# Kernel optimization log

Measured on AMD Instinct MI355X. Metric: run time of the kernel, lower is better.

## Reference

```python
import jax, jax.numpy as jnp
import numpy as np

D_MODEL = 1024

def setup_inputs() -> dict:
    key = jax.random.key(0)
    ks = jax.random.split(key, 7)
    x = jax.random.normal(ks[0], (4, 2048, D_MODEL), dtype=jnp.float32)
    s = 1.0 / np.sqrt(D_MODEL)
    Wq = jax.random.uniform(ks[1], (D_MODEL, D_MODEL), jnp.float32, -s, s)
    bq = jax.random.uniform(ks[2], (D_MODEL,), jnp.float32, -s, s)
    Wk = jax.random.uniform(ks[3], (D_MODEL, D_MODEL), jnp.float32, -s, s)
    bk = jax.random.uniform(ks[4], (D_MODEL,), jnp.float32, -s, s)
    Wv = jax.random.uniform(ks[5], (D_MODEL, D_MODEL), jnp.float32, -s, s)
    bv = jax.random.uniform(ks[6], (D_MODEL,), jnp.float32, -s, s)
    return {"x": x, "Wq": Wq, "bq": bq, "Wk": Wk, "bk": bk, "Wv": Wv, "bv": bv}

def reference(x, Wq, bq, Wk, bk, Wv, bv):
    # single-head self-attention: q,k,v are [B, S, D]
    q = x @ Wq + bq
    k = x @ Wk + bk
    v = x @ Wv + bv
    scale = 1.0 / jnp.sqrt(jnp.asarray(D_MODEL, x.dtype))
    scores = jnp.einsum('bsd,btd->bst', q, k) * scale  # [B, S, S]
    attn = jax.nn.softmax(scores, axis=-1)
    return jnp.einsum('bst,btd->bsd', attn, v)
```

## Files before the change

### kernel.cpp

```cpp
#include <hip/hip_runtime.h>
#include <hip/hip_bf16.h>
#include <stdint.h>


typedef __attribute__((ext_vector_type(8))) short short8;
typedef __attribute__((ext_vector_type(4))) float f32x4;

__device__ __forceinline__ unsigned short f2bf(float f) {
  union { float f; uint32_t u; } c; c.f = f;
  uint32_t u = c.u;
  u += 0x7FFFu + ((u >> 16) & 1u);
  return (unsigned short)(u >> 16);
}

__device__ __forceinline__ void gl16(const void* g, void* l) {
  __builtin_amdgcn_global_load_lds(
      (const __attribute__((address_space(1))) unsigned int*)g,
      (__attribute__((address_space(3))) unsigned int*)l, 16, 0, 0);
}

template <int EPI>
__global__ __launch_bounds__(256) void gemm_bt(
    const short* __restrict__ A, int lda, long sAz,
    const short* __restrict__ B, int ldb, long sBz,
    void* __restrict__ Cv, int ldc, long sCz,
    int K, float scale,
    const float* __restrict__ bias0, const float* __restrict__ bias1,
    const float* __restrict__ bias2, float* __restrict__ rowsum)
{
  __shared__ short lds[18432];
  short* sA = lds;
  short* sB = lds + 8192;

  const int tid  = threadIdx.x;
  const int lane = tid & 63;
  const int wid  = tid >> 6;
  const int z    = blockIdx.z;
  const long tileM = (long)blockIdx.y * 128;
  const long tileN = (long)blockIdx.x * 128;
  const short* Az = A + (long)z * sAz;
  const short* Bz = B + (long)z * sBz;

  const int r0 = wid * 16 + (lane >> 2);
  const int c0 = (lane & 3) * 8;
  const short* gA0 = Az + (tileM + r0) * lda + c0;
  const short* gB0 = Bz + (tileN + r0) * ldb + c0;
  short* lA0 = sA + (wid * 64 + lane) * 8;
  short* lB0 = sB + (wid * 64 + lane) * 8;
  const long a64 = 64L * lda, b64 = 64L * ldb;

  const int fr = lane & 15, quad = lane >> 4;
  const int waveM = (wid >> 1) * 64, waveN = (wid & 1) * 64;

  f32x4 acc[4][4] = {};

  for (int kt = 0; kt < K; kt += 64) {
    __syncthreads();
    gl16(gA0 + kt,             lA0);
    gl16(gA0 + kt + a64,       lA0 + 2048);
    gl16(gA0 + kt + 32,        lA0 + 4096);
    gl16(gA0 + kt + a64 + 32,  lA0 + 6144);
    gl16(gB0 + kt,             lB0);
    gl16(gB0 + kt + b64,       lB0 + 2048);
    gl16(gB0 + kt + 32,        lB0 + 4096);
    gl16(gB0 + kt + b64 + 32,  lB0 + 6144);
    __syncthreads();

#pragma unroll
    for (int kk = 0; kk < 2; ++kk) {
      short8 af[4], bf[4];
#pragma unroll
      for (int i = 0; i < 4; ++i)
        af[i] = *(const short8*)&sA[kk * 4096 + (waveM + i * 16 + fr) * 32 + quad * 8];
#pragma unroll
      for (int j = 0; j < 4; ++j)
        bf[j] = *(const short8*)&sB[kk * 4096 + (waveN + j * 16 + fr) * 32 + quad * 8];
#pragma unroll
      for (int i = 0; i < 4; ++i)
#pragma unroll
        for (int j = 0; j < 4; ++j)
          acc[i][j] = __builtin_amdgcn_mfma_f32_16x16x32_bf16(af[i], bf[j],
                                                              acc[i][j], 0, 0, 0);
    }
  }

  if (EPI == 1) {
#pragma unroll
    for (int i = 0; i < 4; ++i)
#pragma unroll
      for (int j = 0; j < 4; ++j)
#pragma unroll
        for (int r = 0; r < 4; ++r)
          acc[i][j][r] = exp2f(acc[i][j][r] * scale);
#pragma unroll
    for (int i = 0; i < 4; ++i)
#pragma unroll
      for (int r = 0; r < 4; ++r) {
        float s = acc[i][0][r] + acc[i][1][r] + acc[i][2][r] + acc[i][3][r];
        s += __shfl_xor(s, 1);
        s += __shfl_xor(s, 2);
        s += __shfl_xor(s, 4);
        s += __shfl_xor(s, 8);
        if (fr == 0)
          atomicAdd(&rowsum[(long)z * 2048 + tileM + waveM + i * 16 + quad * 4 + r], s);
      }
  }

  if (EPI <= 1) {
    __syncthreads();
    short* scr = lds + wid * 4608;
    short* C = (short*)Cv + (long)z * sCz;
    const float* bias = (z == 0) ? bias0 : ((z == 1) ? bias1 : bias2);
#pragma unroll
    for (int j = 0; j < 4; ++j) {
      const float bv = (EPI == 0) ? bias[tileN + waveN + j * 16 + fr] : 0.0f;
#pragma unroll
      for (int i = 0; i < 4; ++i)
#pragma unroll
        for (int r = 0; r < 4; ++r)
          scr[(i * 16 + quad * 4 + r) * 72 + j * 16 + fr] =
              (short)f2bf(acc[i][j][r] + bv);
    }
    __syncthreads();
#pragma unroll
    for (int c = 0; c < 8; ++c) {
      const int row = c * 8 + (lane >> 3);
      const int col = (lane & 7) * 8;
      short8 v = *(const short8*)&scr[row * 72 + col];
      *(short8*)(C + (tileM + waveM + row) * ldc + tileN + waveN + col) = v;
    }
  } else {
    float* C = (float*)Cv + (long)z * sCz;
#pragma unroll
    for (int i = 0; i < 4; ++i)
#pragma unroll
      for (int r = 0; r < 4; ++r) {
        const long gr = tileM + waveM + i * 16 + quad * 4 + r;
        const float rinv = 1.0f / rowsum[(long)z * 2048 + gr];
#pragma unroll
        for (int j = 0; j < 4; ++j)
          C[gr * ldc + tileN + waveN + j * 16 + fr] = acc[i][j][r] * rinv;
      }
  }
}

__global__ __launch_bounds__(256) void cvt_f32_to_bf16(
    const float4* __restrict__ x, ushort4* __restrict__ y)
{
  const long i = (long)blockIdx.x * 256 + threadIdx.x;
  float4 v = x[i];
  ushort4 o;
  o.x = f2bf(v.x); o.y = f2bf(v.y); o.z = f2bf(v.z); o.w = f2bf(v.w);
  y[i] = o;
}

__global__ __launch_bounds__(256) void transpose_cvt_w(
    const float* __restrict__ Wq, const float* __restrict__ Wk,
    const float* __restrict__ Wv, short* __restrict__ WT)
{
  __shared__ short tile[32][33];
  const int z = blockIdx.z;
  const float* W = (z == 0) ? Wq : ((z == 1) ? Wk : Wv);
  short* d = WT + (long)z * 1024 * 1024;
  const int n0 = blockIdx.x * 32, d0 = blockIdx.y * 32;
  const int tx = threadIdx.x & 31, ty = threadIdx.x >> 5;
#pragma unroll
  for (int p = 0; p < 4; ++p)
    tile[ty + p * 8][tx] = (short)f2bf(W[(long)(d0 + ty + p * 8) * 1024 + n0 + tx]);
  __syncthreads();
#pragma unroll
  for (int p = 0; p < 4; ++p)
    d[(long)(n0 + ty + p * 8) * 1024 + d0 + tx] = tile[tx][ty + p * 8];
}

__global__ __launch_bounds__(256) void transpose_bf16(
    const short* __restrict__ src, short* __restrict__ dst)
{
  __shared__ short tile[32][33];
  const int z = blockIdx.z;
  const int d0 = blockIdx.x * 32, t0 = blockIdx.y * 32;
  const int tx = threadIdx.x & 31, ty = threadIdx.x >> 5;
  const short* s = src + (long)z * 2048 * 1024;
  short* d = dst + (long)z * 1024 * 2048;
#pragma unroll
  for (int p = 0; p < 4; ++p)
    tile[ty + p * 8][tx] = s[(long)(t0 + ty + p * 8) * 1024 + d0 + tx];
  __syncthreads();
#pragma unroll
  for (int p = 0; p < 4; ++p)
    d[(long)(d0 + ty + p * 8) * 2048 + t0 + tx] = tile[tx][ty + p * 8];
}

extern "C" void kernel_launch(void* const* d_in, const int* in_sizes, int n_in,
                              void* d_out, int out_size, void* d_ws, size_t ws_size,
                              hipStream_t stream) {
  const float* x  = (const float*)d_in[0];
  const float* Wq = (const float*)d_in[1];
  const float* bq = (const float*)d_in[2];
  const float* Wk = (const float*)d_in[3];
  const float* bk = (const float*)d_in[4];
  const float* Wv = (const float*)d_in[5];
  const float* bv = (const float*)d_in[6];

  char* ws = (char*)d_ws;
  short* xb  = (short*)(ws);
  short* wt  = (short*)(ws + 16777216);
  short* qkv = (short*)(ws + 23068672);
  short* Pp  = (short*)(ws + 73400320);
  float* rs  = (float*)(ws + 106954752);
  short* vT  = xb;

  hipMemsetAsync(rs, 0, 4 * 2048 * sizeof(float), stream);
  cvt_f32_to_bf16<<<8192, 256, 0, stream>>>((const float4*)x, (ushort4*)xb);
  transpose_cvt_w<<<dim3(32, 32, 3), 256, 0, stream>>>(Wq, Wk, Wv, wt);
  gemm_bt<0><<<dim3(8, 64, 3), 256, 0, stream>>>(
      xb, 1024, 0L, wt, 1024, 1048576L, qkv, 1024, 8388608L,
      1024, 1.0f, bq, bk, bv, nullptr);
  transpose_bf16<<<dim3(32, 64, 4), 256, 0, stream>>>(qkv + 2L * 8388608, vT);
  gemm_bt<1><<<dim3(16, 16, 4), 256, 0, stream>>>(
      qkv, 1024, 2097152L, qkv + 8388608, 1024, 2097152L, Pp, 2048, 4194304L,
      1024, 0.03125f * 1.44269504088896f, nullptr, nullptr, nullptr, rs);
  gemm_bt<2><<<dim3(8, 16, 4), 256, 0, stream>>>(
      Pp, 2048, 4194304L, vT, 2048, 2097152L, d_out, 1024, 2097152L,
      2048, 1.0f, nullptr, nullptr, nullptr, rs);
}
```

Baseline: 299.2 us.

## Double-buffer GEMM LDS tiles and fuse prep kernels into one launch

Restructures the shared GEMM main loop to use two 32-wide K tiles in LDS. The global-to-LDS load for the next tile is issued before the MFMA work on the current one, so each iteration needs only one barrier and load latency can overlap compute. The float-to-bf16 conversion of x, the weight transpose-convert and the rowsum zeroing (previously a memset) are merged into a single prep launch to cut launch overhead. A per-wave epilogue barrier is also dropped. The price is twice as many K iterations, each with less MFMA work between barriers.

```diff
diff --git a/kernel.cpp b/kernel.cpp
--- a/kernel.cpp
+++ b/kernel.cpp
@@ -20,7 +20,7 @@
 }
 
 template <int EPI>
-__global__ __launch_bounds__(256) void gemm_bt(
+__device__ __forceinline__ void gemm_body(
     const short* __restrict__ A, int lda, long sAz,
     const short* __restrict__ B, int ldb, long sBz,
     void* __restrict__ Cv, int ldc, long sCz,
@@ -29,8 +29,6 @@
     const float* __restrict__ bias2, float* __restrict__ rowsum)
 {
   __shared__ short lds[18432];
-  short* sA = lds;
-  short* sB = lds + 8192;
 
   const int tid  = threadIdx.x;
   const int lane = tid & 63;
@@ -41,47 +39,52 @@
   const short* Az = A + (long)z * sAz;
   const short* Bz = B + (long)z * sBz;
 
-  const int r0 = wid * 16 + (lane >> 2);
-  const int c0 = (lane & 3) * 8;
-  const short* gA0 = Az + (tileM + r0) * lda + c0;
-  const short* gB0 = Bz + (tileN + r0) * ldb + c0;
-  short* lA0 = sA + (wid * 64 + lane) * 8;
-  short* lB0 = sB + (wid * 64 + lane) * 8;
-  const long a64 = 64L * lda, b64 = 64L * ldb;
+  const int c0 = tid, c1 = 256 + tid;
+  const short* gA0 = Az + (tileM + (c0 >> 2)) * lda + (c0 & 3) * 8;
+  const short* gA1 = Az + (tileM + (c1 >> 2)) * lda + (c1 & 3) * 8;
+  const short* gB0 = Bz + (tileN + (c0 >> 2)) * ldb + (c0 & 3) * 8;
+  const short* gB1 = Bz + (tileN + (c1 >> 2)) * ldb + (c1 & 3) * 8;
 
   const int fr = lane & 15, quad = lane >> 4;
   const int waveM = (wid >> 1) * 64, waveN = (wid & 1) * 64;
 
   f32x4 acc[4][4] = {};
 
-  for (int kt = 0; kt < K; kt += 64) {
+  const int T = K >> 5;
+
+  {
+    short* base = lds;
+    gl16(gA0, base + c0 * 8);
+    gl16(gA1, base + c1 * 8);
+    gl16(gB0, base + 4096 + c0 * 8);
+    gl16(gB1, base + 4096 + c1 * 8);
+  }
+
+  for (int t = 0; t < T; ++t) {
     __syncthreads();
-    gl16(gA0 + kt,             lA0);
-    gl16(gA0 + kt + a64,       lA0 + 2048);
-    gl16(gA0 + kt + 32,        lA0 + 4096);
-    gl16(gA0 + kt + a64 + 32,  lA0 + 6144);
-    gl16(gB0 + kt,             lB0);
-    gl16(gB0 + kt + b64,       lB0 + 2048);
-    gl16(gB0 + kt + 32,        lB0 + 4096);
-    gl16(gB0 + kt + b64 + 32,  lB0 + 6144);
-    __syncthreads();
-
-#pragma unroll
-    for (int kk = 0; kk < 2; ++kk) {
-      short8 af[4], bf[4];
-#pragma unroll
-      for (int i = 0; i < 4; ++i)
-        af[i] = *(const short8*)&sA[kk * 4096 + (waveM + i * 16 + fr) * 32 + quad * 8];
+    if (t + 1 < T) {
+      const int kt = (t + 1) << 5;
+      short* base = lds + ((t + 1) & 1) * 8192;
+      gl16(gA0 + kt, base + c0 * 8);
+      gl16(gA1 + kt, base + c1 * 8);
+      gl16(gB0 + kt, base + 4096 + c0 * 8);
+      gl16(gB1 + kt, base + 4096 + c1 * 8);
+    }
+    const short* sA = lds + (t & 1) * 8192;
+    const short* sB = sA + 4096;
+    short8 af[4], bf[4];
+#pragma unroll
+    for (int i = 0; i < 4; ++i)
+      af[i] = *(const short8*)&sA[(waveM + i * 16 + fr) * 32 + quad * 8];
+#pragma unroll
+    for (int j = 0; j < 4; ++j)
+      bf[j] = *(const short8*)&sB[(waveN + j * 16 + fr) * 32 + quad * 8];
+#pragma unroll
+    for (int i = 0; i < 4; ++i)
 #pragma unroll
       for (int j = 0; j < 4; ++j)
-        bf[j] = *(const short8*)&sB[kk * 4096 + (waveN + j * 16 + fr) * 32 + quad * 8];
-#pragma unroll
-      for (int i = 0; i < 4; ++i)
-#pragma unroll
-        for (int j = 0; j < 4; ++j)
-          acc[i][j] = __builtin_amdgcn_mfma_f32_16x16x32_bf16(af[i], bf[j],
-                                                              acc[i][j], 0, 0, 0);
-    }
+        acc[i][j] = __builtin_amdgcn_mfma_f32_16x16x32_bf16(af[i], bf[j],
+                                                            acc[i][j], 0, 0, 0);
   }
 
   if (EPI == 1) {
@@ -121,7 +124,6 @@
           scr[(i * 16 + quad * 4 + r) * 72 + j * 16 + fr] =
               (short)f2bf(acc[i][j][r] + bv);
     }
-    __syncthreads();
 #pragma unroll
     for (int c = 0; c < 8; ++c) {
       const int row = c * 8 + (lane >> 3);
@@ -144,33 +146,58 @@
   }
 }
 
-__global__ __launch_bounds__(256) void cvt_f32_to_bf16(
-    const float4* __restrict__ x, ushort4* __restrict__ y)
-{
-  const long i = (long)blockIdx.x * 256 + threadIdx.x;
-  float4 v = x[i];
-  ushort4 o;
-  o.x = f2bf(v.x); o.y = f2bf(v.y); o.z = f2bf(v.z); o.w = f2bf(v.w);
-  y[i] = o;
-}
-
-__global__ __launch_bounds__(256) void transpose_cvt_w(
+__global__ __launch_bounds__(256) void gemm_qkv(
+    const short* A, int lda, long sAz, const short* B, int ldb, long sBz,
+    void* Cv, int ldc, long sCz, int K, float scale,
+    const float* b0, const float* b1, const float* b2, float* rs) {
+  gemm_body<0>(A, lda, sAz, B, ldb, sBz, Cv, ldc, sCz, K, scale, b0, b1, b2, rs);
+}
+__global__ __launch_bounds__(256) void gemm_score(
+    const short* A, int lda, long sAz, const short* B, int ldb, long sBz,
+    void* Cv, int ldc, long sCz, int K, float scale,
+    const float* b0, const float* b1, const float* b2, float* rs) {
+  gemm_body<1>(A, lda, sAz, B, ldb, sBz, Cv, ldc, sCz, K, scale, b0, b1, b2, rs);
+}
+__global__ __launch_bounds__(256) void gemm_pv(
+    const short* A, int lda, long sAz, const short* B, int ldb, long sBz,
+    void* Cv, int ldc, long sCz, int K, float scale,
+    const float* b0, const float* b1, const float* b2, float* rs) {
+  gemm_body<2>(A, lda, sAz, B, ldb, sBz, Cv, ldc, sCz, K, scale, b0, b1, b2, rs);
+}
+
+__global__ __launch_bounds__(256) void prep(
+    const float4* __restrict__ x, ushort4* __restrict__ xb,
     const float* __restrict__ Wq, const float* __restrict__ Wk,
-    const float* __restrict__ Wv, short* __restrict__ WT)
+    const float* __restrict__ Wv, short* __restrict__ WT,
+    float* __restrict__ rs)
 {
   __shared__ short tile[32][33];
-  const int z = blockIdx.z;
-  const float* W = (z == 0) ? Wq : ((z == 1) ? Wk : Wv);
-  short* d = WT + (long)z * 1024 * 1024;
-  const int n0 = blockIdx.x * 32, d0 = blockIdx.y * 32;
-  const int tx = threadIdx.x & 31, ty = threadIdx.x >> 5;
-#pragma unroll
-  for (int p = 0; p < 4; ++p)
-    tile[ty + p * 8][tx] = (short)f2bf(W[(long)(d0 + ty + p * 8) * 1024 + n0 + tx]);
-  __syncthreads();
-#pragma unroll
-  for (int p = 0; p < 4; ++p)
-    d[(long)(n0 + ty + p * 8) * 1024 + d0 + tx] = tile[tx][ty + p * 8];
+  const int b = blockIdx.x;
+  if (b < 8192) {
+    const long i = (long)b * 256 + threadIdx.x;
+    float4 v = x[i];
+    ushort4 o;
+    o.x = f2bf(v.x); o.y = f2bf(v.y); o.z = f2bf(v.z); o.w = f2bf(v.w);
+    xb[i] = o;
+  } else if (b < 11264) {
+    const int idx = b - 8192;
+    const int z = idx >> 10, rem = idx & 1023;
+    const float* W = (z == 0) ? Wq : ((z == 1) ? Wk : Wv);
+    short* d = WT + (long)z * 1024 * 1024;
+    const int n0 = (rem & 31) * 32, d0 = (rem >> 5) * 32;
+    const int tx = threadIdx.x & 31, ty = threadIdx.x >> 5;
+#pragma unroll
+    for (int p = 0; p < 4; ++p)
+      tile[ty + p * 8][tx] = (short)f2bf(W[(long)(d0 + ty + p * 8) * 1024 + n0 + tx]);
+    __syncthreads();
+#pragma unroll
+    for (int p = 0; p < 4; ++p)
+      d[(long)(n0 + ty + p * 8) * 1024 + d0 + tx] = tile[tx][ty + p * 8];
+  } else {
+#pragma unroll
+    for (int p = 0; p < 32; ++p)
+      rs[p * 256 + threadIdx.x] = 0.0f;
+  }
 }
 
 __global__ __launch_bounds__(256) void transpose_bf16(
@@ -210,17 +237,16 @@
   float* rs  = (float*)(ws + 106954752);
   short* vT  = xb;
 
-  hipMemsetAsync(rs, 0, 4 * 2048 * sizeof(float), stream);
-  cvt_f32_to_bf16<<<8192, 256, 0, stream>>>((const float4*)x, (ushort4*)xb);
-  transpose_cvt_w<<<dim3(32, 32, 3), 256, 0, stream>>>(Wq, Wk, Wv, wt);
-  gemm_bt<0><<<dim3(8, 64, 3), 256, 0, stream>>>(
+  prep<<<11265, 256, 0, stream>>>((const float4*)x, (ushort4*)xb,
+                                  Wq, Wk, Wv, wt, rs);
+  gemm_qkv<<<dim3(8, 64, 3), 256, 0, stream>>>(
       xb, 1024, 0L, wt, 1024, 1048576L, qkv, 1024, 8388608L,
       1024, 1.0f, bq, bk, bv, nullptr);
   transpose_bf16<<<dim3(32, 64, 4), 256, 0, stream>>>(qkv + 2L * 8388608, vT);
-  gemm_bt<1><<<dim3(16, 16, 4), 256, 0, stream>>>(
+  gemm_score<<<dim3(16, 16, 4), 256, 0, stream>>>(
       qkv, 1024, 2097152L, qkv + 8388608, 1024, 2097152L, Pp, 2048, 4194304L,
       1024, 0.03125f * 1.44269504088896f, nullptr, nullptr, nullptr, rs);
-  gemm_bt<2><<<dim3(8, 16, 4), 256, 0, stream>>>(
+  gemm_pv<<<dim3(8, 16, 4), 256, 0, stream>>>(
       Pp, 2048, 4194304L, vT, 2048, 2097152L, d_out, 1024, 2097152L,
       2048, 1.0f, nullptr, nullptr, nullptr, rs);
 }
```

After: 275.0 us. 8.1% less time.
